# Kernel tuning notes

Measured on AMD Instinct MI355X. Metric: run time of the kernel, lower is better.

The kernel has to match this reference:

```python
import jax, jax.numpy as jnp
import numpy as np

N = 150000      # active voxels
C = 64          # head input channels
KK = 9          # 3x3 kernel offsets
H = W = 700     # BEV feature map
BN_EPS = 1e-5
HEADS = [("heatmap", 3), ("center", 2), ("center_z", 1), ("dim", 3), ("rot", 2)]


def _build_neighbor_table(seed=0):
    """Submanifold 3x3 neighbor indices for N active voxels on an HxW grid.
    Entry -1 means the neighbor site is inactive (contributes zero)."""
    rng = np.random.default_rng(seed)
    flat = rng.choice(H * W, size=N, replace=False)
    ys, xs = flat // W, flat % W
    lut = np.full(H * W, -1, np.int64)
    lut[flat] = np.arange(N)
    nbr = np.full((N, KK), -1, np.int64)
    k = 0
    for dy in (-1, 0, 1):
        for dx in (-1, 0, 1):
            ny, nx = ys + dy, xs + dx
            valid = (ny >= 0) & (ny < H) & (nx >= 0) & (nx < W)
            nf = np.where(valid, ny * W + nx, 0)
            nbr[:, k] = np.where(valid, lut[nf], -1)
            k += 1
    return nbr


def setup_inputs() -> dict:
    key = jax.random.key(0)
    ks = jax.random.split(key, 2 + 2 * len(HEADS))
    inp = {
        "features": jax.random.normal(ks[0], (N, C), jnp.float32),
        "nbr_idx": jnp.asarray(_build_neighbor_table(), jnp.int32),
        # one 3x3 subm conv per head, stacked: [n_heads, 9, C_in, C_out]
        "W3": jax.random.normal(ks[1], (len(HEADS), KK, C, C), jnp.float32) * 0.05,
        "gamma": jnp.ones((len(HEADS), C), jnp.float32),
        "beta": jnp.zeros((len(HEADS), C), jnp.float32),
    }
    for i, (name, oc) in enumerate(HEADS):
        inp[f"W1_{name}"] = jax.random.normal(ks[2 + i], (C, oc), jnp.float32) * 0.001
        if name == "heatmap":
            inp[f"b1_{name}"] = jnp.full((oc,), -float(np.log((1 - 0.01) / 0.01)), jnp.float32)
        else:
            inp[f"b1_{name}"] = jnp.zeros((oc,), jnp.float32)
    return inp


def _forward(features, nbr_idx, W3, gamma, beta, W1s, b1s):
    valid = nbr_idx >= 0                                  # [N, 9]
    idx = jnp.where(valid, nbr_idx, 0)
    # gather active-neighbor features; missing neighbors -> zero (subm conv)
    gathered = features[idx] * valid[..., None].astype(features.dtype)  # [N, 9, C]
    # all heads share the same input sparse tensor -> batched gather-GEMM
    h = jnp.einsum('nkc,hkco->hno', gathered, W3)         # [n_heads, N, C]
    # BatchNorm1d (training-mode batch stats, biased var) + ReLU
    mean = h.mean(axis=1, keepdims=True)
    var = ((h - mean) ** 2).mean(axis=1, keepdims=True)
    hn = (h - mean) * jax.lax.rsqrt(var + BN_EPS)
    hn = jax.nn.relu(hn * gamma[:, None, :] + beta[:, None, :])
    # per-head 1x1 subm conv == linear on active features
    return tuple(hn[i] @ W1s[i] + b1s[i] for i in range(len(HEADS)))


def reference(features, nbr_idx, W3, gamma, beta,
              W1_heatmap, b1_heatmap, W1_center, b1_center,
              W1_center_z, b1_center_z, W1_dim, b1_dim, W1_rot, b1_rot):
    W1s = [W1_heatmap, W1_center, W1_center_z, W1_dim, W1_rot]
    b1s = [b1_heatmap, b1_center, b1_center_z, b1_dim, b1_rot]
    return _forward(features, nbr_idx, W3, gamma, beta, W1s, b1s)
```

## Files before the change

### kernel.cpp

```cpp
#include <hip/hip_runtime.h>

#define NVOX 150000
#define BM 128
#define MTILES 1172
#define SROW 150016
#define NCOL 320

typedef __attribute__((ext_vector_type(8))) short bf16x8;
typedef __attribute__((ext_vector_type(4))) float f32x4;
typedef __attribute__((ext_vector_type(4))) unsigned short us4;

__device__ __forceinline__ unsigned short f2bf(float f) {
    unsigned u = __builtin_bit_cast(unsigned, f);
    u += 0x7fffu + ((u >> 16) & 1u);
    return (unsigned short)(u >> 16);
}

__device__ __forceinline__ void gld16(const void* g, void* l) {
    __builtin_amdgcn_global_load_lds(
        (const __attribute__((address_space(1))) unsigned int*)g,
        (__attribute__((address_space(3))) unsigned int*)l, 16, 0, 0);
}

__global__ void prep_feat(const float* __restrict__ src, unsigned short* __restrict__ dst) {
    int i = blockIdx.x * 256 + threadIdx.x;
    if (i < NVOX * 8) {
        const float4 a = *(const float4*)(src + (size_t)i * 8);
        const float4 b = *(const float4*)(src + (size_t)i * 8 + 4);
        us4 lo, hi;
        lo.x = f2bf(a.x); lo.y = f2bf(a.y); lo.z = f2bf(a.z); lo.w = f2bf(a.w);
        hi.x = f2bf(b.x); hi.y = f2bf(b.y); hi.z = f2bf(b.z); hi.w = f2bf(b.w);
        *(us4*)(dst + (size_t)i * 8) = lo;
        *(us4*)(dst + (size_t)i * 8 + 4) = hi;
    } else if (i < NVOX * 8 + 8) {
        us4 z; z.x = 0; z.y = 0; z.z = 0; z.w = 0;
        *(us4*)(dst + (size_t)i * 8) = z;
    }
}

__global__ void prep_w3(const float* __restrict__ w3, unsigned short* __restrict__ bf,
                        float* __restrict__ stats) {
    __shared__ float tile[64 * 65];
    int b = blockIdx.x;
    int tid = threadIdx.x;
    const float* src = w3 + (size_t)b * 4096;
#pragma unroll
    for (int t = 0; t < 16; ++t) {
        int lin = t * 256 + tid;
        tile[(lin >> 6) * 65 + (lin & 63)] = src[lin];
    }
    __syncthreads();
    int h = b / 9, kk = b - h * 9;
    unsigned short* dst = bf + (size_t)(kk * 5 + h) * 4096;
#pragma unroll
    for (int t = 0; t < 16; ++t) {
        int lin = t * 256 + tid;
        int e = lin & 7;
        int lane = (lin >> 3) & 63;
        int t2 = lin >> 9;
        int c = (t2 >> 2) * 32 + (lane >> 4) * 8 + e;
        int o = (t2 & 3) * 16 + (lane & 15);
        dst[lin] = f2bf(tile[c * 65 + o]);
    }
    if (b == 0) for (int j = tid; j < 2 * NCOL; j += 256) stats[j] = 0.f;
}

__global__ __launch_bounds__(256, 2)
void gemm_kernel(const unsigned short* __restrict__ featB,
                 const unsigned short* __restrict__ Bf,
                 const int* __restrict__ nbr,
                 unsigned short* __restrict__ hbuf,
                 float* __restrict__ stats) {
    __shared__ __align__(16) char smem[38400];
    constexpr int IDX_OFF = 32768;
    constexpr int SRED_OFF = 37376;

    int mtile = blockIdx.x;
    int m0 = mtile * BM;
    int tid = threadIdx.x;
    int w = tid >> 6, lane = tid & 63;
    int quad = lane >> 4, m16 = lane & 15;
    int mrow = (w >> 1) * 64;
    int colhalf = w & 1;

    for (int lin = tid; lin < 1152; lin += 256) {
        int kkq = lin >> 7, row = lin & 127;
        int v = (m0 + row < NVOX) ? nbr[(size_t)(m0 + row) * 9 + kkq] : -1;
        *(int*)(smem + IDX_OFF + lin * 4) = ((v < 0) ? NVOX : v) * 128;
    }
    __syncthreads();

    f32x4 acc[5][4][2];
#pragma unroll
    for (int h = 0; h < 5; ++h)
#pragma unroll
        for (int mt = 0; mt < 4; ++mt)
#pragma unroll
            for (int nt = 0; nt < 2; ++nt)
                acc[h][mt][nt] = (f32x4){0.f, 0.f, 0.f, 0.f};

    const char* fb = (const char*)featB;
    const char* bfb = (const char*)Bf + colhalf * 2048 + lane * 16;

#define STAGE(kkx)                                                              \
    do {                                                                        \
        int o0 = *(const int*)(smem + IDX_OFF + ((kkx) * 128 + lane) * 4);      \
        int o1 = *(const int*)(smem + IDX_OFF + ((kkx) * 128 + 64 + lane) * 4); \
        char* dstS = smem + ((kkx) & 1) * 16384;                                \
        int cA = w * 2, cB = w * 2 + 1;                                         \
        gld16(fb + o0 + cA * 16, dstS + cA * 2048);                             \
        gld16(fb + o1 + cA * 16, dstS + cA * 2048 + 1024);                      \
        gld16(fb + o0 + cB * 16, dstS + cB * 2048);                             \
        gld16(fb + o1 + cB * 16, dstS + cB * 2048 + 1024);                      \
    } while (0)

#define LDB(dst, kkx, h)                                                        \
    do {                                                                        \
        _Pragma("unroll")                                                       \
        for (int ks = 0; ks < 2; ++ks)                                          \
            _Pragma("unroll")                                                   \
            for (int nt = 0; nt < 2; ++nt)                                      \
                dst[ks * 2 + nt] = *(const bf16x8*)(bfb +                       \
                    ((kkx) * 5 + (h)) * 8192 + ks * 4096 + nt * 1024);          \
    } while (0)

#define MFH(h, B)                                                               \
    do {                                                                        \
        _Pragma("unroll")                                                       \
        for (int ks = 0; ks < 2; ++ks)                                          \
            _Pragma("unroll")                                                   \
            for (int mt = 0; mt < 4; ++mt)                                      \
                _Pragma("unroll")                                               \
                for (int nt = 0; nt < 2; ++nt)                                  \
                    acc[h][mt][nt] = __builtin_amdgcn_mfma_f32_16x16x32_bf16(   \
                        af[ks][mt], B[ks * 2 + nt], acc[h][mt][nt], 0, 0, 0);   \
    } while (0)

    STAGE(0);
    for (int kk = 0; kk < 9; ++kk) {
        __syncthreads();
        const char* cur = smem + (kk & 1) * 16384;
        bf16x8 af[2][4];
#pragma unroll
        for (int ks = 0; ks < 2; ++ks)
#pragma unroll
            for (int mt = 0; mt < 4; ++mt)
                af[ks][mt] = *(const bf16x8*)(cur + (ks * 4 + quad) * 2048 +
                                              (mrow + mt * 16 + m16) * 16);
        bf16x8 ba[4], bb[4];
        LDB(ba, kk, 0);
        LDB(bb, kk, 1);
        if (kk < 8) STAGE(kk + 1);
        MFH(0, ba); LDB(ba, kk, 2);
        MFH(1, bb); LDB(bb, kk, 3);
        MFH(2, ba); LDB(ba, kk, 4);
        MFH(3, bb);
        MFH(4, ba);
    }
    __syncthreads();
#undef STAGE
#undef LDB
#undef MFH

    unsigned short* sOut = (unsigned short*)smem;
    float2* sRed = (float2*)(smem + SRED_OFF);
#pragma unroll
    for (int h = 0; h < 5; ++h) {
        float s[2], ss[2];
#pragma unroll
        for (int nt = 0; nt < 2; ++nt) {
            int col = colhalf * 32 + nt * 16 + m16;
            float a = 0.f, b = 0.f;
#pragma unroll
            for (int mt = 0; mt < 4; ++mt) {
                int row = mrow + mt * 16 + quad * 4;
                f32x4 v = acc[h][mt][nt];
                unsigned lo = (unsigned)f2bf(v.x) | ((unsigned)f2bf(v.y) << 16);
                unsigned hi = (unsigned)f2bf(v.z) | ((unsigned)f2bf(v.w) << 16);
                uint2 pk; pk.x = lo; pk.y = hi;
                *(uint2*)(sOut + col * 136 + row) = pk;
                a += v.x + v.y + v.z + v.w;
                b += v.x * v.x + v.y * v.y + v.z * v.z + v.w * v.w;
            }
            s[nt] = a; ss[nt] = b;
            s[nt] += __shfl_xor(s[nt], 16); s[nt] += __shfl_xor(s[nt], 32);
            ss[nt] += __shfl_xor(ss[nt], 16); ss[nt] += __shfl_xor(ss[nt], 32);
        }
        if (quad == 0) {
#pragma unroll
            for (int nt = 0; nt < 2; ++nt) {
                float2 p; p.x = s[nt]; p.y = ss[nt];
                sRed[(w * 2 + nt) * 16 + m16] = p;
            }
        }
        __syncthreads();
#pragma unroll
        for (int it = 0; it < 8; ++it) {
            int col = it * 8 + (tid >> 5);
            int l32 = tid & 31;
            uint2 v = *(const uint2*)(sOut + col * 136 + l32 * 4);
            *(uint2*)(hbuf + (size_t)(h * 64 + col) * SROW + m0 + l32 * 4) = v;
        }
        if (tid < 64) {
            int ch = tid >> 5, nt = (tid >> 4) & 1, mc = tid & 15;
            float2 p0 = sRed[((ch) * 2 + nt) * 16 + mc];
            float2 p1 = sRed[((ch + 2) * 2 + nt) * 16 + mc];
            atomicAdd(&stats[h * 64 + tid], p0.x + p1.x);
            atomicAdd(&stats[NCOL + h * 64 + tid], p0.y + p1.y);
        }
        __syncthreads();
    }
}

__global__ void head_kernel(const unsigned short* __restrict__ hbuf,
                            const float* __restrict__ stats,
                            const float* __restrict__ gamma, const float* __restrict__ beta,
                            const float* __restrict__ W1_0, const float* __restrict__ W1_1,
                            const float* __restrict__ W1_2, const float* __restrict__ W1_3,
                            const float* __restrict__ W1_4,
                            const float* __restrict__ b1_0, const float* __restrict__ b1_1,
                            const float* __restrict__ b1_2, const float* __restrict__ b1_3,
                            const float* __restrict__ b1_4,
                            float* __restrict__ out) {
    __shared__ float sScale[NCOL], sShift[NCOL], sW1[NCOL * 3], sB1[16];
    int tid = threadIdx.x;
    for (int c = tid; c < NCOL; c += 256) {
        float mean = stats[c] * (1.f / (float)NVOX);
        float var = stats[NCOL + c] * (1.f / (float)NVOX) - mean * mean;
        float inv = rsqrtf(var + 1e-5f);
        float sc = inv * gamma[c];
        sScale[c] = sc;
        sShift[c] = beta[c] - mean * sc;
    }
    for (int i = tid; i < 192; i += 256) { int cc = i / 3, jj = i - cc * 3; sW1[0 * 192 + i] = W1_0[cc * 3 + jj]; }
    for (int i = tid; i < 192; i += 256) { int cc = i / 3, jj = i - cc * 3; sW1[1 * 192 + i] = (jj < 2) ? W1_1[cc * 2 + jj] : 0.f; }
    for (int i = tid; i < 192; i += 256) { int cc = i / 3, jj = i - cc * 3; sW1[2 * 192 + i] = (jj < 1) ? W1_2[cc] : 0.f; }
    for (int i = tid; i < 192; i += 256) { int cc = i / 3, jj = i - cc * 3; sW1[3 * 192 + i] = W1_3[cc * 3 + jj]; }
    for (int i = tid; i < 192; i += 256) { int cc = i / 3, jj = i - cc * 3; sW1[4 * 192 + i] = (jj < 2) ? W1_4[cc * 2 + jj] : 0.f; }
    if (tid == 0) {
        sB1[0] = b1_0[0]; sB1[1] = b1_0[1]; sB1[2] = b1_0[2];
        sB1[3] = b1_1[0]; sB1[4] = b1_1[1]; sB1[5] = 0.f;
        sB1[6] = b1_2[0]; sB1[7] = 0.f;    sB1[8] = 0.f;
        sB1[9] = b1_3[0]; sB1[10] = b1_3[1]; sB1[11] = b1_3[2];
        sB1[12] = b1_4[0]; sB1[13] = b1_4[1]; sB1[14] = 0.f;
    }
    __syncthreads();
    int lin = blockIdx.x * 256 + tid;
    int h = lin / 75008;
    int rp = lin - h * 75008;
    if (rp >= 75000) return;
    int n = rp * 2;
    const unsigned short* hp = hbuf + n;
    float x0 = sB1[h * 3 + 0], x1 = sB1[h * 3 + 1], x2 = sB1[h * 3 + 2];
    float y0 = x0, y1 = x1, y2 = x2;
    int cbase = h * 64;
#pragma unroll 16
    for (int cc = 0; cc < 64; ++cc) {
        int c = cbase + cc;
        unsigned raw = *(const unsigned*)(hp + (size_t)c * SROW);
        float v0 = __builtin_bit_cast(float, raw << 16);
        float v1 = __builtin_bit_cast(float, raw & 0xffff0000u);
        float sc = sScale[c], sh = sShift[c];
        v0 = fmaxf(v0 * sc + sh, 0.f);
        v1 = fmaxf(v1 * sc + sh, 0.f);
        float w0 = sW1[c * 3 + 0], w1 = sW1[c * 3 + 1], w2 = sW1[c * 3 + 2];
        x0 += v0 * w0; x1 += v0 * w1; x2 += v0 * w2;
        y0 += v1 * w0; y1 += v1 * w1; y2 += v1 * w2;
    }
    if (h == 0) {
        out[n * 3 + 0] = x0; out[n * 3 + 1] = x1; out[n * 3 + 2] = x2;
        out[(n + 1) * 3 + 0] = y0; out[(n + 1) * 3 + 1] = y1; out[(n + 1) * 3 + 2] = y2;
    } else if (h == 1) {
        out[450000 + n * 2 + 0] = x0; out[450000 + n * 2 + 1] = x1;
        out[450000 + (n + 1) * 2 + 0] = y0; out[450000 + (n + 1) * 2 + 1] = y1;
    } else if (h == 2) {
        out[750000 + n] = x0; out[750000 + n + 1] = y0;
    } else if (h == 3) {
        out[900000 + n * 3 + 0] = x0; out[900000 + n * 3 + 1] = x1; out[900000 + n * 3 + 2] = x2;
        out[900000 + (n + 1) * 3 + 0] = y0; out[900000 + (n + 1) * 3 + 1] = y1; out[900000 + (n + 1) * 3 + 2] = y2;
    } else {
        out[1350000 + n * 2 + 0] = x0; out[1350000 + n * 2 + 1] = x1;
        out[1350000 + (n + 1) * 2 + 0] = y0; out[1350000 + (n + 1) * 2 + 1] = y1;
    }
}

extern "C" void kernel_launch(void* const* d_in, const int* in_sizes, int n_in,
                              void* d_out, int out_size, void* d_ws, size_t ws_size,
                              hipStream_t stream) {
    const float* features = (const float*)d_in[0];
    const int* nbr        = (const int*)d_in[1];
    const float* w3       = (const float*)d_in[2];
    const float* gamma    = (const float*)d_in[3];
    const float* beta     = (const float*)d_in[4];
    const float* W1_0 = (const float*)d_in[5];  const float* b1_0 = (const float*)d_in[6];
    const float* W1_1 = (const float*)d_in[7];  const float* b1_1 = (const float*)d_in[8];
    const float* W1_2 = (const float*)d_in[9];  const float* b1_2 = (const float*)d_in[10];
    const float* W1_3 = (const float*)d_in[11]; const float* b1_3 = (const float*)d_in[12];
    const float* W1_4 = (const float*)d_in[13]; const float* b1_4 = (const float*)d_in[14];
    float* out = (float*)d_out;

    char* ws = (char*)d_ws;
    unsigned short* featB = (unsigned short*)ws;
    unsigned short* Bf    = (unsigned short*)(ws + 19200128);
    float* stats          = (float*)(ws + 19568768);
    unsigned short* hbuf  = (unsigned short*)(ws + 19571328);

    prep_feat<<<(NVOX * 8 + 8 + 255) / 256, 256, 0, stream>>>(features, featB);
    prep_w3<<<45, 256, 0, stream>>>(w3, Bf, stats);
    gemm_kernel<<<MTILES, 256, 0, stream>>>(featB, Bf, nbr, hbuf, stats);
    head_kernel<<<(5 * 75008) / 256, 256, 0, stream>>>(hbuf, stats, gamma, beta,
        W1_0, W1_1, W1_2, W1_3, W1_4, b1_0, b1_1, b1_2, b1_3, b1_4, out);
}
```

Measured before the change: 237.4 us.

## Restructure gather-GEMM to one wave per head with 64-row tiles

The gather-GEMM now uses 64-row tiles and 5 waves per block, each wave owning one head's full 64 output columns, instead of 4 waves splitting rows and column halves across all five heads. This cuts the per-thread accumulator from 40 to 16 MFMA tiles, aiming for more resident blocks per CU (launch bounds 320,4) and better latency hiding on the random neighbour gathers. Each wave now loads its own head's B fragments, stats go directly to global atomics, and output is written per head with wider 16-byte stores. In exchange, the gathered A tile is shared across fewer rows, atomic traffic on the stats doubles, and there are more blocks and barriers per row.

New measurement: 255.0 us. 7.4% more time.

```diff
diff --git a/kernel.cpp b/kernel.cpp
--- a/kernel.cpp
+++ b/kernel.cpp
@@ -1,8 +1,8 @@
 #include <hip/hip_runtime.h>
 
 #define NVOX 150000
-#define BM 128
-#define MTILES 1172
+#define BM 64
+#define MTILES 2344
 #define SROW 150016
 #define NCOL 320
 
@@ -65,120 +65,128 @@
     if (b == 0) for (int j = tid; j < 2 * NCOL; j += 256) stats[j] = 0.f;
 }
 
-__global__ __launch_bounds__(256, 2)
+__global__ __launch_bounds__(320, 4)
 void gemm_kernel(const unsigned short* __restrict__ featB,
                  const unsigned short* __restrict__ Bf,
                  const int* __restrict__ nbr,
                  unsigned short* __restrict__ hbuf,
                  float* __restrict__ stats) {
-    __shared__ __align__(16) char smem[38400];
-    constexpr int IDX_OFF = 32768;
-    constexpr int SRED_OFF = 37376;
+    __shared__ __align__(16) char smem[18688];
+    constexpr int IDX_OFF = 16384;
 
     int mtile = blockIdx.x;
     int m0 = mtile * BM;
     int tid = threadIdx.x;
     int w = tid >> 6, lane = tid & 63;
     int quad = lane >> 4, m16 = lane & 15;
-    int mrow = (w >> 1) * 64;
-    int colhalf = w & 1;
-
-    for (int lin = tid; lin < 1152; lin += 256) {
-        int kkq = lin >> 7, row = lin & 127;
-        int v = (m0 + row < NVOX) ? nbr[(size_t)(m0 + row) * 9 + kkq] : -1;
-        *(int*)(smem + IDX_OFF + lin * 4) = ((v < 0) ? NVOX : v) * 128;
+    int* sIdx = (int*)(smem + IDX_OFF);
+
+    for (int lin = tid; lin < 576; lin += 320) {
+        int v = (m0 * 9 + lin < NVOX * 9) ? nbr[(size_t)m0 * 9 + lin] : -1;
+        int row = lin / 9, kkq = lin - row * 9;
+        sIdx[kkq * 64 + row] = ((v < 0) ? NVOX : v) * 128;
     }
     __syncthreads();
 
-    f32x4 acc[5][4][2];
-#pragma unroll
-    for (int h = 0; h < 5; ++h)
-#pragma unroll
-        for (int mt = 0; mt < 4; ++mt)
-#pragma unroll
-            for (int nt = 0; nt < 2; ++nt)
-                acc[h][mt][nt] = (f32x4){0.f, 0.f, 0.f, 0.f};
+    f32x4 acc[4][4];
+#pragma unroll
+    for (int mt = 0; mt < 4; ++mt)
+#pragma unroll
+        for (int nt = 0; nt < 4; ++nt)
+            acc[mt][nt] = (f32x4){0.f, 0.f, 0.f, 0.f};
 
     const char* fb = (const char*)featB;
-    const char* bfb = (const char*)Bf + colhalf * 2048 + lane * 16;
+    const char* bq = (const char*)Bf + (size_t)w * 8192 + lane * 16;
 
 #define STAGE(kkx)                                                              \
     do {                                                                        \
-        int o0 = *(const int*)(smem + IDX_OFF + ((kkx) * 128 + lane) * 4);      \
-        int o1 = *(const int*)(smem + IDX_OFF + ((kkx) * 128 + 64 + lane) * 4); \
-        char* dstS = smem + ((kkx) & 1) * 16384;                                \
-        int cA = w * 2, cB = w * 2 + 1;                                         \
-        gld16(fb + o0 + cA * 16, dstS + cA * 2048);                             \
-        gld16(fb + o1 + cA * 16, dstS + cA * 2048 + 1024);                      \
-        gld16(fb + o0 + cB * 16, dstS + cB * 2048);                             \
-        gld16(fb + o1 + cB * 16, dstS + cB * 2048 + 1024);                      \
+        if (w < 4) {                                                            \
+            int off = sIdx[(kkx) * 64 + lane];                                  \
+            char* dstS = smem + ((kkx) & 1) * 8192;                             \
+            gld16(fb + off + (w * 2) * 16, dstS + (w * 2) * 1024);              \
+            gld16(fb + off + (w * 2 + 1) * 16, dstS + (w * 2 + 1) * 1024);      \
+        }                                                                       \
     } while (0)
 
-#define LDB(dst, kkx, h)                                                        \
-    do {                                                                        \
-        _Pragma("unroll")                                                       \
-        for (int ks = 0; ks < 2; ++ks)                                          \
-            _Pragma("unroll")                                                   \
-            for (int nt = 0; nt < 2; ++nt)                                      \
-                dst[ks * 2 + nt] = *(const bf16x8*)(bfb +                       \
-                    ((kkx) * 5 + (h)) * 8192 + ks * 4096 + nt * 1024);          \
-    } while (0)
-
-#define MFH(h, B)                                                               \
-    do {                                                                        \
-        _Pragma("unroll")                                                       \
-        for (int ks = 0; ks < 2; ++ks)                                          \
-            _Pragma("unroll")                                                   \
-            for (int mt = 0; mt < 4; ++mt)                                      \
-                _Pragma("unroll")                                               \
-                for (int nt = 0; nt < 2; ++nt)                                  \
-                    acc[h][mt][nt] = __builtin_amdgcn_mfma_f32_16x16x32_bf16(   \
-                        af[ks][mt], B[ks * 2 + nt], acc[h][mt][nt], 0, 0, 0);   \
-    } while (0)
-
     STAGE(0);
+#pragma unroll
     for (int kk = 0; kk < 9; ++kk) {
         __syncthreads();
-        const char* cur = smem + (kk & 1) * 16384;
-        bf16x8 af[2][4];
-#pragma unroll
-        for (int ks = 0; ks < 2; ++ks)
-#pragma unroll
-            for (int mt = 0; mt < 4; ++mt)
-                af[ks][mt] = *(const bf16x8*)(cur + (ks * 4 + quad) * 2048 +
-                                              (mrow + mt * 16 + m16) * 16);
-        bf16x8 ba[4], bb[4];
-        LDB(ba, kk, 0);
-        LDB(bb, kk, 1);
+        const char* cur = smem + (kk & 1) * 8192;
+        bf16x8 b0[4], b1[4];
+#pragma unroll
+        for (int nt = 0; nt < 4; ++nt)
+            b0[nt] = *(const bf16x8*)(bq + (kk * 5) * 8192 + (0 * 4 + nt) * 1024);
+#pragma unroll
+        for (int nt = 0; nt < 4; ++nt)
+            b1[nt] = *(const bf16x8*)(bq + (kk * 5) * 8192 + (1 * 4 + nt) * 1024);
         if (kk < 8) STAGE(kk + 1);
-        MFH(0, ba); LDB(ba, kk, 2);
-        MFH(1, bb); LDB(bb, kk, 3);
-        MFH(2, ba); LDB(ba, kk, 4);
-        MFH(3, bb);
-        MFH(4, ba);
-    }
+        {
+            bf16x8 af[4];
+#pragma unroll
+            for (int mt = 0; mt < 4; ++mt)
+                af[mt] = *(const bf16x8*)(cur + quad * 1024 + (mt * 16 + m16) * 16);
+#pragma unroll
+            for (int mt = 0; mt < 4; ++mt)
+#pragma unroll
+                for (int nt = 0; nt < 4; ++nt)
+                    acc[mt][nt] = __builtin_amdgcn_mfma_f32_16x16x32_bf16(
+                        af[mt], b0[nt], acc[mt][nt], 0, 0, 0);
+        }
+        {
+            bf16x8 af[4];
+#pragma unroll
+            for (int mt = 0; mt < 4; ++mt)
+                af[mt] = *(const bf16x8*)(cur + (4 + quad) * 1024 + (mt * 16 + m16) * 16);
+#pragma unroll
+            for (int mt = 0; mt < 4; ++mt)
+#pragma unroll
+                for (int nt = 0; nt < 4; ++nt)
+                    acc[mt][nt] = __builtin_amdgcn_mfma_f32_16x16x32_bf16(
+                        af[mt], b1[nt], acc[mt][nt], 0, 0, 0);
+        }
+    }
+#undef STAGE
     __syncthreads();
-#undef STAGE
-#undef LDB
-#undef MFH
 
     unsigned short* sOut = (unsigned short*)smem;
-    float2* sRed = (float2*)(smem + SRED_OFF);
 #pragma unroll
     for (int h = 0; h < 5; ++h) {
-        float s[2], ss[2];
-#pragma unroll
-        for (int nt = 0; nt < 2; ++nt) {
-            int col = colhalf * 32 + nt * 16 + m16;
+        if (w == h) {
+#pragma unroll
+            for (int mt = 0; mt < 4; ++mt)
+#pragma unroll
+                for (int nt = 0; nt < 4; ++nt) {
+                    int col = nt * 16 + m16;
+                    int row = mt * 16 + quad * 4;
+                    f32x4 v = acc[mt][nt];
+                    unsigned lo = (unsigned)f2bf(v.x) | ((unsigned)f2bf(v.y) << 16);
+                    unsigned hi = (unsigned)f2bf(v.z) | ((unsigned)f2bf(v.w) << 16);
+                    uint2 pk; pk.x = lo; pk.y = hi;
+                    *(uint2*)(sOut + col * 136 + row) = pk;
+                }
+        }
+        __syncthreads();
+        if (tid < 256) {
+#pragma unroll
+            for (int it = 0; it < 2; ++it) {
+                int s = it * 256 + tid;
+                int col = s >> 3, l8 = s & 7;
+                uint4 v = *(const uint4*)(sOut + col * 136 + l8 * 8);
+                *(uint4*)(hbuf + (size_t)(h * 64 + col) * SROW + m0 + l8 * 8) = v;
+            }
+        }
+        __syncthreads();
+    }
+
+    {
+        float s[4], ss[4];
+#pragma unroll
+        for (int nt = 0; nt < 4; ++nt) {
             float a = 0.f, b = 0.f;
 #pragma unroll
             for (int mt = 0; mt < 4; ++mt) {
-                int row = mrow + mt * 16 + quad * 4;
-                f32x4 v = acc[h][mt][nt];
-                unsigned lo = (unsigned)f2bf(v.x) | ((unsigned)f2bf(v.y) << 16);
-                unsigned hi = (unsigned)f2bf(v.z) | ((unsigned)f2bf(v.w) << 16);
-                uint2 pk; pk.x = lo; pk.y = hi;
-                *(uint2*)(sOut + col * 136 + row) = pk;
+                f32x4 v = acc[mt][nt];
                 a += v.x + v.y + v.z + v.w;
                 b += v.x * v.x + v.y * v.y + v.z * v.z + v.w * v.w;
             }
@@ -188,27 +196,11 @@
         }
         if (quad == 0) {
 #pragma unroll
-            for (int nt = 0; nt < 2; ++nt) {
-                float2 p; p.x = s[nt]; p.y = ss[nt];
-                sRed[(w * 2 + nt) * 16 + m16] = p;
+            for (int nt = 0; nt < 4; ++nt) {
+                atomicAdd(&stats[w * 64 + nt * 16 + m16], s[nt]);
+                atomicAdd(&stats[NCOL + w * 64 + nt * 16 + m16], ss[nt]);
             }
         }
-        __syncthreads();
-#pragma unroll
-        for (int it = 0; it < 8; ++it) {
-            int col = it * 8 + (tid >> 5);
-            int l32 = tid & 31;
-            uint2 v = *(const uint2*)(sOut + col * 136 + l32 * 4);
-            *(uint2*)(hbuf + (size_t)(h * 64 + col) * SROW + m0 + l32 * 4) = v;
-        }
-        if (tid < 64) {
-            int ch = tid >> 5, nt = (tid >> 4) & 1, mc = tid & 15;
-            float2 p0 = sRed[((ch) * 2 + nt) * 16 + mc];
-            float2 p1 = sRed[((ch + 2) * 2 + nt) * 16 + mc];
-            atomicAdd(&stats[h * 64 + tid], p0.x + p1.x);
-            atomicAdd(&stats[NCOL + h * 64 + tid], p0.y + p1.y);
-        }
-        __syncthreads();
     }
 }
 
@@ -307,7 +299,7 @@
 
     prep_feat<<<(NVOX * 8 + 8 + 255) / 256, 256, 0, stream>>>(features, featB);
     prep_w3<<<45, 256, 0, stream>>>(w3, Bf, stats);
-    gemm_kernel<<<MTILES, 256, 0, stream>>>(featB, Bf, nbr, hbuf, stats);
+    gemm_kernel<<<MTILES, 320, 0, stream>>>(featB, Bf, nbr, hbuf, stats);
     head_kernel<<<(5 * 75008) / 256, 256, 0, stream>>>(hbuf, stats, gamma, beta,
         W1_0, W1_1, W1_2, W1_3, W1_4, b1_0, b1_1, b1_2, b1_3, b1_4, out);
 }
```

## Split GEMM heads across two block types and re-layout gathered A tile

Applied to the files above, without the earlier changes.

Each M-tile is now handled by two blocks: one computes heads 0-2 and the other heads 3-4. Block IDs are interleaved so the two blocks for a tile run close together and can share the gathered rows in L2. This cuts the per-block accumulator footprint from 5 heads to 3 and doubles the grid, aiming for better occupancy and latency hiding. The shared-memory A tile moves from a channel-chunk-major layout to a row-major layout, with matching gather and read addressing. In exchange, neighbor gathers and index loads are duplicated across the two blocks, and the 3-head and 2-head blocks carry unequal work.

Result: slower. 561.9 us (+136.7%).

```diff
diff --git a/kernel.cpp b/kernel.cpp
--- a/kernel.cpp
+++ b/kernel.cpp
@@ -75,24 +75,32 @@
     constexpr int IDX_OFF = 32768;
     constexpr int SRED_OFF = 37376;
 
-    int mtile = blockIdx.x;
+    int bid = blockIdx.x;
+    int r = bid & 7, q = bid >> 3;
+    int type = q & 1;
+    int mtile = (q >> 1) * 8 + r;
+    if (mtile >= MTILES) return;
+    int h0 = type ? 3 : 0;
+    int nh = type ? 2 : 3;
     int m0 = mtile * BM;
+
     int tid = threadIdx.x;
     int w = tid >> 6, lane = tid & 63;
     int quad = lane >> 4, m16 = lane & 15;
     int mrow = (w >> 1) * 64;
     int colhalf = w & 1;
+    int* sIdx = (int*)(smem + IDX_OFF);
 
     for (int lin = tid; lin < 1152; lin += 256) {
         int kkq = lin >> 7, row = lin & 127;
         int v = (m0 + row < NVOX) ? nbr[(size_t)(m0 + row) * 9 + kkq] : -1;
-        *(int*)(smem + IDX_OFF + lin * 4) = ((v < 0) ? NVOX : v) * 128;
+        sIdx[lin] = ((v < 0) ? NVOX : v) * 128;
     }
     __syncthreads();
 
-    f32x4 acc[5][4][2];
-#pragma unroll
-    for (int h = 0; h < 5; ++h)
+    f32x4 acc[3][4][2];
+#pragma unroll
+    for (int h = 0; h < 3; ++h)
 #pragma unroll
         for (int mt = 0; mt < 4; ++mt)
 #pragma unroll
@@ -100,72 +108,59 @@
                 acc[h][mt][nt] = (f32x4){0.f, 0.f, 0.f, 0.f};
 
     const char* fb = (const char*)featB;
-    const char* bfb = (const char*)Bf + colhalf * 2048 + lane * 16;
-
+    const char* bp = (const char*)Bf + h0 * 8192 + colhalf * 2048 + lane * 16;
+
+    int r16 = lane >> 2, c4 = lane & 3;
 #define STAGE(kkx)                                                              \
     do {                                                                        \
-        int o0 = *(const int*)(smem + IDX_OFF + ((kkx) * 128 + lane) * 4);      \
-        int o1 = *(const int*)(smem + IDX_OFF + ((kkx) * 128 + 64 + lane) * 4); \
-        char* dstS = smem + ((kkx) & 1) * 16384;                                \
-        int cA = w * 2, cB = w * 2 + 1;                                         \
-        gld16(fb + o0 + cA * 16, dstS + cA * 2048);                             \
-        gld16(fb + o1 + cA * 16, dstS + cA * 2048 + 1024);                      \
-        gld16(fb + o0 + cB * 16, dstS + cB * 2048);                             \
-        gld16(fb + o1 + cB * 16, dstS + cB * 2048 + 1024);                      \
-    } while (0)
-
-#define LDB(dst, kkx, h)                                                        \
-    do {                                                                        \
-        _Pragma("unroll")                                                       \
-        for (int ks = 0; ks < 2; ++ks)                                          \
-            _Pragma("unroll")                                                   \
-            for (int nt = 0; nt < 2; ++nt)                                      \
-                dst[ks * 2 + nt] = *(const bf16x8*)(bfb +                       \
-                    ((kkx) * 5 + (h)) * 8192 + ks * 4096 + nt * 1024);          \
-    } while (0)
-
-#define MFH(h, B)                                                               \
-    do {                                                                        \
-        _Pragma("unroll")                                                       \
-        for (int ks = 0; ks < 2; ++ks)                                          \
-            _Pragma("unroll")                                                   \
-            for (int mt = 0; mt < 4; ++mt)                                      \
-                _Pragma("unroll")                                               \
-                for (int nt = 0; nt < 2; ++nt)                                  \
-                    acc[h][mt][nt] = __builtin_amdgcn_mfma_f32_16x16x32_bf16(   \
-                        af[ks][mt], B[ks * 2 + nt], acc[h][mt][nt], 0, 0, 0);   \
+        char* dstS = smem + ((kkx) & 1) * 16384 + w * 2048;                     \
+        int offA = sIdx[(kkx) * 128 + w * 32 + r16];                            \
+        int offB = sIdx[(kkx) * 128 + w * 32 + 16 + r16];                       \
+        gld16(fb + offA + c4 * 16, dstS);                                       \
+        gld16(fb + offB + c4 * 16, dstS + 1024);                                \
+        gld16(fb + offA + 64 + c4 * 16, dstS + 8192);                           \
+        gld16(fb + offB + 64 + c4 * 16, dstS + 8192 + 1024);                    \
     } while (0)
 
     STAGE(0);
     for (int kk = 0; kk < 9; ++kk) {
         __syncthreads();
         const char* cur = smem + (kk & 1) * 16384;
-        bf16x8 af[2][4];
+        bf16x8 bfr[2][3][2];
 #pragma unroll
         for (int ks = 0; ks < 2; ++ks)
 #pragma unroll
+            for (int h = 0; h < 3; ++h)
+                if (h < nh)
+#pragma unroll
+                    for (int nt = 0; nt < 2; ++nt)
+                        bfr[ks][h][nt] = *(const bf16x8*)(bp + ks * 4096 + h * 8192 + nt * 1024);
+        if (kk < 8) STAGE(kk + 1);
+#pragma unroll
+        for (int ks = 0; ks < 2; ++ks) {
+            bf16x8 af[4];
+#pragma unroll
             for (int mt = 0; mt < 4; ++mt)
-                af[ks][mt] = *(const bf16x8*)(cur + (ks * 4 + quad) * 2048 +
-                                              (mrow + mt * 16 + m16) * 16);
-        bf16x8 ba[4], bb[4];
-        LDB(ba, kk, 0);
-        LDB(bb, kk, 1);
-        if (kk < 8) STAGE(kk + 1);
-        MFH(0, ba); LDB(ba, kk, 2);
-        MFH(1, bb); LDB(bb, kk, 3);
-        MFH(2, ba); LDB(ba, kk, 4);
-        MFH(3, bb);
-        MFH(4, ba);
-    }
+                af[mt] = *(const bf16x8*)(cur + ks * 8192 +
+                                          (mrow + mt * 16 + m16) * 64 + quad * 16);
+#pragma unroll
+            for (int h = 0; h < 3; ++h)
+                if (h < nh)
+#pragma unroll
+                    for (int mt = 0; mt < 4; ++mt)
+#pragma unroll
+                        for (int nt = 0; nt < 2; ++nt)
+                            acc[h][mt][nt] = __builtin_amdgcn_mfma_f32_16x16x32_bf16(
+                                af[mt], bfr[ks][h][nt], acc[h][mt][nt], 0, 0, 0);
+        }
+        bp += 40960;
+    }
+#undef STAGE
     __syncthreads();
-#undef STAGE
-#undef LDB
-#undef MFH
 
     unsigned short* sOut = (unsigned short*)smem;
-    float2* sRed = (float2*)(smem + SRED_OFF);
-#pragma unroll
-    for (int h = 0; h < 5; ++h) {
+    float* sRed = (float*)(smem + SRED_OFF);
+    for (int h = 0; h < nh; ++h) {
         float s[2], ss[2];
 #pragma unroll
         for (int nt = 0; nt < 2; ++nt) {
@@ -189,8 +184,8 @@
         if (quad == 0) {
 #pragma unroll
             for (int nt = 0; nt < 2; ++nt) {
-                float2 p; p.x = s[nt]; p.y = ss[nt];
-                sRed[(w * 2 + nt) * 16 + m16] = p;
+                sRed[((w * 2 + nt) * 16 + m16) * 2 + 0] = s[nt];
+                sRed[((w * 2 + nt) * 16 + m16) * 2 + 1] = ss[nt];
             }
         }
         __syncthreads();
@@ -199,14 +194,16 @@
             int col = it * 8 + (tid >> 5);
             int l32 = tid & 31;
             uint2 v = *(const uint2*)(sOut + col * 136 + l32 * 4);
-            *(uint2*)(hbuf + (size_t)(h * 64 + col) * SROW + m0 + l32 * 4) = v;
+            *(uint2*)(hbuf + (size_t)((h0 + h) * 64 + col) * SROW + m0 + l32 * 4) = v;
         }
         if (tid < 64) {
             int ch = tid >> 5, nt = (tid >> 4) & 1, mc = tid & 15;
-            float2 p0 = sRed[((ch) * 2 + nt) * 16 + mc];
-            float2 p1 = sRed[((ch + 2) * 2 + nt) * 16 + mc];
-            atomicAdd(&stats[h * 64 + tid], p0.x + p1.x);
-            atomicAdd(&stats[NCOL + h * 64 + tid], p0.y + p1.y);
+            float a = sRed[((ch * 2 + nt) * 16 + mc) * 2 + 0] +
+                      sRed[(((ch + 2) * 2 + nt) * 16 + mc) * 2 + 0];
+            float b = sRed[((ch * 2 + nt) * 16 + mc) * 2 + 1] +
+                      sRed[(((ch + 2) * 2 + nt) * 16 + mc) * 2 + 1];
+            atomicAdd(&stats[(h0 + h) * 64 + tid], a);
+            atomicAdd(&stats[NCOL + (h0 + h) * 64 + tid], b);
         }
         __syncthreads();
     }
@@ -307,7 +304,7 @@
 
     prep_feat<<<(NVOX * 8 + 8 + 255) / 256, 256, 0, stream>>>(features, featB);
     prep_w3<<<45, 256, 0, stream>>>(w3, Bf, stats);
-    gemm_kernel<<<MTILES, 256, 0, stream>>>(featB, Bf, nbr, hbuf, stats);
+    gemm_kernel<<<8 * 2 * 147, 256, 0, stream>>>(featB, Bf, nbr, hbuf, stats);
     head_kernel<<<(5 * 75008) / 256, 256, 0, stream>>>(hbuf, stats, gamma, beta,
         W1_0, W1_1, W1_2, W1_3, W1_4, b1_0, b1_1, b1_2, b1_3, b1_4, out);
 }
```
